# Optimization experiments

Hardware: AMD Instinct MI355X
Metric: run time of the kernel (lower is better)

Reference implementation:

```python
import jax, jax.numpy as jnp
import numpy as np

N_EVENTS = 16
N_SAMPLES = 2 ** 15  # 32768


def fft_shift(stems, shift_samples):
    """Fractionally shift each atom in time via frequency-domain phase rotation.
    stems: (B, E, N) float32; shift_samples: (B, E) float32 in [0, N].
    """
    n = stems.shape[-1]
    freqs = jnp.fft.rfftfreq(n).astype(jnp.float32)  # (n//2+1,) cycles/sample
    theta = 2.0 * jnp.pi * freqs[None, None, :] * shift_samples[..., None]  # (B,E,F)
    phase = jnp.cos(theta) - 1j * jnp.sin(theta)  # exp(-i*theta)
    spec = jnp.fft.rfft(stems, axis=-1)
    return jnp.fft.irfft(spec * phase, n=n, axis=-1)


def setup_inputs() -> dict:
    key = jax.random.key(0)
    k1, k2, k3, k4 = jax.random.split(key, 4)
    B = 64
    time_latent = jax.random.normal(k1, (B, N_EVENTS, 128), dtype=jnp.float32)
    stems = jax.random.normal(k2, (B, N_EVENTS, N_SAMPLES), dtype=jnp.float32)
    targets = jax.random.normal(k3, (B, 1, N_SAMPLES), dtype=jnp.float32)
    W_pos = jax.random.normal(k4, (1, 128), dtype=jnp.float32) * 0.1
    b_pos = jnp.zeros((1,), dtype=jnp.float32)
    return {"time_latent": time_latent, "stems": stems, "targets": targets,
            "W_pos": W_pos, "b_pos": b_pos}


def reference(time_latent, stems, targets, W_pos, b_pos):
    # to_pos: Linear(128 -> 1), then sigmoid -> fractional positions in [0,1]
    pos = jax.nn.sigmoid(jnp.einsum('bed,od->beo', time_latent, W_pos) + b_pos)
    pos = pos.reshape(-1, N_EVENTS)  # (B, E)
    # schedule_atoms: place each stem at fractional offset pos * n_samples, sum events
    shifted = fft_shift(stems, pos * N_SAMPLES)  # (B, E, N)
    scheduled = jnp.sum(shifted, axis=1, keepdims=True)  # (B, 1, N), same shape as targets
    return scheduled
```

## Files before the change

kernel.cpp:

```cpp
#include <hip/hip_runtime.h>
#include <math.h>

#define NS      32768
#define M       16384
#define NEV     16
#define NB      64
#define T2      1024

__device__ __forceinline__ int ldsIdx(int i) { return i + (i >> 5) + (i >> 10); }
#define LDS_ELEMS (M + M / 32 + M / 1024)

__device__ __forceinline__ float2 cmul(float2 a, float2 b) {
    return make_float2(a.x * b.x - a.y * b.y, a.x * b.y + a.y * b.x);
}

__device__ __forceinline__ int rev4_14(int i) {
    int r = 0;
#pragma unroll
    for (int d = 0; d < 7; ++d) { r = (r << 2) | (i & 3); i >>= 2; }
    return r;
}

__device__ __forceinline__ float2 shift_phase(int k, int si, float sf) {
    unsigned ksi = ((unsigned)k * (unsigned)si) & (unsigned)(NS - 1);
    float total = (float)ksi + (float)k * sf;
    float f = total * (1.0f / (float)NS);
    f -= floorf(f);
    float ang = -6.28318530717958647692f * f;
    float sv, cv;
    __sincosf(ang, &sv, &cv);
    return make_float2(cv, sv);
}

__device__ __forceinline__ float2 wNS(int k) {
    float ang = (float)k * (-6.28318530717958647692f / (float)NS);
    float sv, cv;
    __sincosf(ang, &sv, &cv);
    return make_float2(cv, sv);
}

__device__ __constant__ float R16C[4] = {1.0f, 0.92387953251128675613f,
                                         0.70710678118654752440f, 0.38268343236508977173f};
__device__ __constant__ float R16S[4] = {0.0f, 0.38268343236508977173f,
                                         0.70710678118654752440f, 0.92387953251128675613f};

__device__ __constant__ float C32[16] = {
    1.0f, 0.98078528040323044913f, 0.92387953251128675613f, 0.83146961230254523708f,
    0.70710678118654752440f, 0.55557023301960222474f, 0.38268343236508977173f,
    0.19509032201612826785f, 0.0f, -0.19509032201612826785f, -0.38268343236508977173f,
    -0.55557023301960222474f, -0.70710678118654752440f, -0.83146961230254523708f,
    -0.92387953251128675613f, -0.98078528040323044913f};
__device__ __constant__ float S32[16] = {
    0.0f, 0.19509032201612826785f, 0.38268343236508977173f, 0.55557023301960222474f,
    0.70710678118654752440f, 0.83146961230254523708f, 0.92387953251128675613f,
    0.98078528040323044913f, 1.0f, 0.98078528040323044913f, 0.92387953251128675613f,
    0.83146961230254523708f, 0.70710678118654752440f, 0.55557023301960222474f,
    0.38268343236508977173f, 0.19509032201612826785f};

template <int SIGN>
__device__ void fft_lds(float2* lds, int tid) {
    const float TP = (SIGN < 0) ? -6.28318530717958647692f
                                :  6.28318530717958647692f;
#pragma unroll
    for (int tp = 0; tp < 3; ++tp) {
        const int t = 2 * tp;
        const int q = 1 << (2 * t);
        const int j = tid & (q - 1);
        const int base = ((tid >> (2 * t)) << (2 * t + 4)) + j;
        float2 x[16];
#pragma unroll
        for (int l = 0; l < 16; ++l) x[l] = lds[ldsIdx(base + l * q)];

        float2 ww, w1, w2, w3;
        if (tp > 0) {
            float sv, cv;
            __sincosf(TP * (float)j / (float)(16 * q), &sv, &cv);
            ww = make_float2(cv, sv);
            float2 s2 = cmul(ww, ww);
            w1 = cmul(s2, s2);
            w2 = cmul(w1, w1);
            w3 = cmul(w2, w1);
        }

#pragma unroll
        for (int m = 0; m < 4; ++m) {
            float2 a0 = x[4 * m], a1 = x[4 * m + 1], a2 = x[4 * m + 2], a3 = x[4 * m + 3];
            if (tp > 0) { a1 = cmul(a1, w1); a2 = cmul(a2, w2); a3 = cmul(a3, w3); }
            float2 u0 = make_float2(a0.x + a2.x, a0.y + a2.y);
            float2 u1 = make_float2(a0.x - a2.x, a0.y - a2.y);
            float2 u2 = make_float2(a1.x + a3.x, a1.y + a3.y);
            float2 u3 = make_float2(a1.x - a3.x, a1.y - a3.y);
            x[4 * m]     = make_float2(u0.x + u2.x, u0.y + u2.y);
            x[4 * m + 2] = make_float2(u0.x - u2.x, u0.y - u2.y);
            if (SIGN < 0) {
                x[4 * m + 1] = make_float2(u1.x + u3.y, u1.y - u3.x);
                x[4 * m + 3] = make_float2(u1.x - u3.y, u1.y + u3.x);
            } else {
                x[4 * m + 1] = make_float2(u1.x - u3.y, u1.y + u3.x);
                x[4 * m + 3] = make_float2(u1.x + u3.y, u1.y - u3.x);
            }
        }

#pragma unroll
        for (int n = 0; n < 4; ++n) {
            float2 a0 = x[n], a1 = x[n + 4], a2 = x[n + 8], a3 = x[n + 12];
            if (!(tp == 0 && n == 0)) {
                float2 r = make_float2(R16C[n], (SIGN < 0) ? -R16S[n] : R16S[n]);
                float2 wp = (tp > 0) ? ((n > 0) ? cmul(ww, r) : ww) : r;
                float2 wp2 = cmul(wp, wp);
                float2 wp3 = cmul(wp2, wp);
                a1 = cmul(a1, wp);
                a2 = cmul(a2, wp2);
                a3 = cmul(a3, wp3);
            }
            float2 u0 = make_float2(a0.x + a2.x, a0.y + a2.y);
            float2 u1 = make_float2(a0.x - a2.x, a0.y - a2.y);
            float2 u2 = make_float2(a1.x + a3.x, a1.y + a3.y);
            float2 u3 = make_float2(a1.x - a3.x, a1.y - a3.y);
            x[n]      = make_float2(u0.x + u2.x, u0.y + u2.y);
            x[n + 8]  = make_float2(u0.x - u2.x, u0.y - u2.y);
            if (SIGN < 0) {
                x[n + 4]  = make_float2(u1.x + u3.y, u1.y - u3.x);
                x[n + 12] = make_float2(u1.x - u3.y, u1.y + u3.x);
            } else {
                x[n + 4]  = make_float2(u1.x - u3.y, u1.y + u3.x);
                x[n + 12] = make_float2(u1.x + u3.y, u1.y - u3.x);
            }
        }
#pragma unroll
        for (int l = 0; l < 16; ++l) lds[ldsIdx(base + l * q)] = x[l];
        __syncthreads();
    }

    {
        const int q = 4096;
        const float c = TP / (float)(4 * q);
        float sv, cv;
        __sincosf(c * (float)tid, &sv, &cv);
        const float2 w1b = make_float2(cv, sv);
#pragma unroll
        for (int it = 0; it < (M / 4) / T2; ++it) {
            const int j = tid + it * T2;
            float2 w1;
            if (it == 0) w1 = w1b;
            else {
                float2 rot = make_float2(R16C[it], (SIGN < 0) ? -R16S[it] : R16S[it]);
                w1 = cmul(w1b, rot);
            }
            float2 w2 = cmul(w1, w1);
            float2 w3 = cmul(w2, w1);
            const int I0 = ldsIdx(j);
            const int I1 = ldsIdx(j + q);
            const int I2 = ldsIdx(j + 2 * q);
            const int I3 = ldsIdx(j + 3 * q);
            float2 a0 = lds[I0];
            float2 a1 = cmul(lds[I1], w1);
            float2 a2 = cmul(lds[I2], w2);
            float2 a3 = cmul(lds[I3], w3);
            float2 u0 = make_float2(a0.x + a2.x, a0.y + a2.y);
            float2 u1 = make_float2(a0.x - a2.x, a0.y - a2.y);
            float2 u2 = make_float2(a1.x + a3.x, a1.y + a3.y);
            float2 u3 = make_float2(a1.x - a3.x, a1.y - a3.y);
            lds[I0] = make_float2(u0.x + u2.x, u0.y + u2.y);
            lds[I2] = make_float2(u0.x - u2.x, u0.y - u2.y);
            if (SIGN < 0) {
                lds[I1] = make_float2(u1.x + u3.y, u1.y - u3.x);
                lds[I3] = make_float2(u1.x - u3.y, u1.y + u3.x);
            } else {
                lds[I1] = make_float2(u1.x - u3.y, u1.y + u3.x);
                lds[I3] = make_float2(u1.x + u3.y, u1.y - u3.x);
            }
        }
        __syncthreads();
    }
}

__global__ __launch_bounds__(64) void pos_kernel(const float* __restrict__ tl,
                                                 const float* __restrict__ W,
                                                 const float* __restrict__ bp,
                                                 float* __restrict__ shifts) {
    int bid = blockIdx.x;
    int t = threadIdx.x;
    const float* row = tl + (size_t)bid * 128;
    float p = row[t] * W[t] + row[t + 64] * W[t + 64];
#pragma unroll
    for (int off = 32; off > 0; off >>= 1) p += __shfl_down(p, off);
    if (t == 0) {
        float x = p + bp[0];
        float sig = 1.0f / (1.0f + expf(-x));
        shifts[bid] = sig * (float)NS;
    }
}

__global__ __launch_bounds__(T2) void fft_phase_kernel(float* __restrict__ stems,
                                                       const float* __restrict__ shifts) {
    __shared__ float2 lds[LDS_ELEMS];
    const int tid = threadIdx.x;
    const int row = blockIdx.x;

    float* rowp = stems + (size_t)row * NS;
    const float4* src = (const float4*)rowp;
#pragma unroll
    for (int it = 0; it < (M / 2) / T2; ++it) {
        int i = tid + it * T2;
        float4 v = src[i];
        lds[ldsIdx(rev4_14(2 * i))]     = make_float2(v.x, v.y);
        lds[ldsIdx(rev4_14(2 * i + 1))] = make_float2(v.z, v.w);
    }
    __syncthreads();

    fft_lds<-1>(lds, tid);

    const float s = shifts[row];
    const int si = (int)floorf(s);
    const float sf = s - (float)si;
    float2* spec = (float2*)rowp;

    const float2 ph0 = shift_phase(tid, si, sf);
    const float2 w0  = wNS(tid);
    const float2 q1  = shift_phase(1024, si, sf);
    const float2 q2  = cmul(q1, q1);
    const float2 q3  = cmul(q2, q1);
    const float2 q4  = cmul(q2, q2);
    float2 phb = ph0;
#pragma unroll
    for (int t = 0; t < M / T2; ++t) {
        int k = tid + (t << 10);
        float2 ph;
        switch (t & 3) {
            case 0:  ph = phb; break;
            case 1:  ph = cmul(phb, q1); break;
            case 2:  ph = cmul(phb, q2); break;
            default: ph = cmul(phb, q3); break;
        }
        if (k == 0) {
            float2 z0 = lds[ldsIdx(0)];
            float X0 = z0.x + z0.y;
            float XM = z0.x - z0.y;
            float2 phM = shift_phase(M, si, sf);
            spec[0] = make_float2(X0, XM * phM.x);
        } else {
            float2 Zk = lds[ldsIdx(k)];
            float2 Zr = lds[ldsIdx(M - k)];
            float2 E = make_float2(0.5f * (Zk.x + Zr.x), 0.5f * (Zk.y - Zr.y));
            float2 O = make_float2(0.5f * (Zk.y + Zr.y), -0.5f * (Zk.x - Zr.x));
            float2 w = cmul(w0, make_float2(C32[t], -S32[t]));
            float2 wo = cmul(w, O);
            float2 X = make_float2(E.x + wo.x, E.y + wo.y);
            spec[k] = cmul(X, ph);
        }
        if ((t & 3) == 3) phb = cmul(phb, q4);
    }
}

__global__ __launch_bounds__(256) void reduce_kernel(const float4* __restrict__ stems,
                                                     float4* __restrict__ out) {
    int gid = blockIdx.x * 256 + threadIdx.x;
    int b = gid >> 13;
    int i = gid & (NS / 4 - 1);
    const float4* base = stems + (size_t)b * NEV * (NS / 4) + i;
    float4 s = base[0];
#pragma unroll
    for (int e = 1; e < NEV; ++e) {
        float4 v = base[(size_t)e * (NS / 4)];
        s.x += v.x; s.y += v.y; s.z += v.z; s.w += v.w;
    }
    out[gid] = s;
}

__global__ __launch_bounds__(T2) void inv_kernel(float* __restrict__ out) {
    __shared__ float2 lds[LDS_ELEMS];
    const int tid = threadIdx.x;
    const int b = blockIdx.x;

    const float4* src = (const float4*)(out + (size_t)b * NS);
#pragma unroll
    for (int it = 0; it < (M / 2) / T2; ++it) {
        int i = tid + it * T2;
        float4 v = src[i];
        lds[ldsIdx(rev4_14(2 * i))]     = make_float2(v.x, v.y);
        lds[ldsIdx(rev4_14(2 * i + 1))] = make_float2(v.z, v.w);
    }
    __syncthreads();

    const float2 w0 = wNS(tid);
#pragma unroll
    for (int t = 0; t < (M / 2) / T2; ++t) {
        int k = tid + (t << 10);
        if (k == 0) {
            float2 a0 = lds[ldsIdx(0)];
            lds[ldsIdx(0)] = make_float2(0.5f * (a0.x + a0.y), 0.5f * (a0.x - a0.y));
            int rh = ldsIdx(rev4_14(M / 2));
            float2 ah = lds[rh];
            lds[rh] = make_float2(ah.x, -ah.y);
        } else {
            int pk = ldsIdx(rev4_14(k));
            int pm = ldsIdx(rev4_14(M - k));
            float2 a = lds[pk];
            float2 bb = lds[pm];
            float2 w = cmul(w0, make_float2(C32[t], -S32[t]));
            float2 E1 = make_float2(0.5f * (a.x + bb.x), 0.5f * (a.y - bb.y));
            float2 D1 = make_float2(0.5f * (a.x - bb.x), 0.5f * (a.y + bb.y));
            float2 wc = make_float2(w.x, -w.y);
            float2 O1 = cmul(wc, D1);
            float2 z1 = make_float2(E1.x - O1.y, E1.y + O1.x);
            float2 E2 = make_float2(E1.x, -E1.y);
            float2 D2 = make_float2(-D1.x, D1.y);
            float2 O2 = cmul(w, D2);
            O2 = make_float2(-O2.x, -O2.y);
            float2 z2 = make_float2(E2.x - O2.y, E2.y + O2.x);
            lds[pk] = z1;
            lds[pm] = z2;
        }
    }
    __syncthreads();

    fft_lds<1>(lds, tid);

    const float invM = 1.0f / (float)M;
    float4* dst = (float4*)(out + (size_t)b * NS);
#pragma unroll
    for (int it = 0; it < (NS / 4) / T2; ++it) {
        int i = tid + it * T2;
        float2 z0 = lds[ldsIdx(2 * i)];
        float2 z1 = lds[ldsIdx(2 * i + 1)];
        dst[i] = make_float4(z0.x * invM, z0.y * invM, z1.x * invM, z1.y * invM);
    }
}

extern "C" void kernel_launch(void* const* d_in, const int* in_sizes, int n_in,
                              void* d_out, int out_size, void* d_ws, size_t ws_size,
                              hipStream_t stream) {
    const float* time_latent = (const float*)d_in[0];
    float* stems = (float*)d_in[1];
    const float* W_pos = (const float*)d_in[3];
    const float* b_pos = (const float*)d_in[4];
    float* out = (float*)d_out;

    float* shifts = (float*)d_ws;

    pos_kernel<<<NB * NEV, 64, 0, stream>>>(time_latent, W_pos, b_pos, shifts);
    fft_phase_kernel<<<NB * NEV, T2, 0, stream>>>(stems, shifts);
    reduce_kernel<<<(NB * NS / 4) / 256, 256, 0, stream>>>((const float4*)stems,
                                                           (float4*)out);
    inv_kernel<<<NB, T2, 0, stream>>>(out);
}
```

Baseline: 296.6 us.

## Fuse pos into FFT kernel, fold first radix-4 stage into load, move repack into reduce

The position linear layer and sigmoid are computed inside the forward FFT kernel, which removes one launch and the round trip of shifts through global memory. The first radix-4 stage is done in registers during the global load and bit-reversed scatter, so the FFT runs as three radix-16 passes instead of three radix-16 passes plus a separate radix-4 LDS pass. The inverse real-FFT pre-twiddle (z-pair repack) moves out of the inverse kernel, which runs only 64 blocks, and into the reduce kernel, which also reads mirrored elements from global memory. In exchange the reduce kernel does strided mirrored reads, and the restructured FFT stage ordering must stay correct.

```diff
diff --git a/kernel.cpp b/kernel.cpp
--- a/kernel.cpp
+++ b/kernel.cpp
@@ -58,12 +58,52 @@
     0.38268343236508977173f, 0.19509032201612826785f};
 
 template <int SIGN>
-__device__ void fft_lds(float2* lds, int tid) {
+__device__ __forceinline__ void btf4(float2* a) {
+    float2 a0 = a[0], a1 = a[1], a2 = a[2], a3 = a[3];
+    float2 u0 = make_float2(a0.x + a2.x, a0.y + a2.y);
+    float2 u1 = make_float2(a0.x - a2.x, a0.y - a2.y);
+    float2 u2 = make_float2(a1.x + a3.x, a1.y + a3.y);
+    float2 u3 = make_float2(a1.x - a3.x, a1.y - a3.y);
+    a[0] = make_float2(u0.x + u2.x, u0.y + u2.y);
+    a[2] = make_float2(u0.x - u2.x, u0.y - u2.y);
+    if (SIGN < 0) {
+        a[1] = make_float2(u1.x + u3.y, u1.y - u3.x);
+        a[3] = make_float2(u1.x - u3.y, u1.y + u3.x);
+    } else {
+        a[1] = make_float2(u1.x - u3.y, u1.y + u3.x);
+        a[3] = make_float2(u1.x + u3.y, u1.y - u3.x);
+    }
+}
+
+template <int SIGN>
+__device__ __forceinline__ void load_stage0_scatter(const float4* __restrict__ src,
+                                                    float2* lds, int tid) {
+    const int R = rev4_14(2 * tid);
+    float2 g0[4], g1[4], g2[4], g3[4];
+#pragma unroll
+    for (int it = 0; it < 8; ++it) {
+        float4 v = src[tid + (it << 10)];
+        int l = it >> 1;
+        if ((it & 1) == 0) { g0[l] = make_float2(v.x, v.y); g1[l] = make_float2(v.z, v.w); }
+        else               { g2[l] = make_float2(v.x, v.y); g3[l] = make_float2(v.z, v.w); }
+    }
+    btf4<SIGN>(g0); btf4<SIGN>(g1); btf4<SIGN>(g2); btf4<SIGN>(g3);
+#pragma unroll
+    for (int l = 0; l < 4; ++l) {
+        lds[ldsIdx(R + l)]               = g0[l];
+        lds[ldsIdx(R + 4096 + l)]        = g1[l];
+        lds[ldsIdx(R + 8 + l)]           = g2[l];
+        lds[ldsIdx(R + 8 + 4096 + l)]    = g3[l];
+    }
+}
+
+template <int SIGN>
+__device__ void fft_pairs(float2* lds, int tid) {
     const float TP = (SIGN < 0) ? -6.28318530717958647692f
                                 :  6.28318530717958647692f;
 #pragma unroll
     for (int tp = 0; tp < 3; ++tp) {
-        const int t = 2 * tp;
+        const int t = 2 * tp + 1;
         const int q = 1 << (2 * t);
         const int j = tid & (q - 1);
         const int base = ((tid >> (2 * t)) << (2 * t + 4)) + j;
@@ -71,21 +111,18 @@
 #pragma unroll
         for (int l = 0; l < 16; ++l) x[l] = lds[ldsIdx(base + l * q)];
 
-        float2 ww, w1, w2, w3;
-        if (tp > 0) {
-            float sv, cv;
-            __sincosf(TP * (float)j / (float)(16 * q), &sv, &cv);
-            ww = make_float2(cv, sv);
-            float2 s2 = cmul(ww, ww);
-            w1 = cmul(s2, s2);
-            w2 = cmul(w1, w1);
-            w3 = cmul(w2, w1);
-        }
+        float sv, cv;
+        __sincosf(TP * (float)j / (float)(16 * q), &sv, &cv);
+        float2 ww = make_float2(cv, sv);
+        float2 s2 = cmul(ww, ww);
+        float2 w1 = cmul(s2, s2);
+        float2 w2 = cmul(w1, w1);
+        float2 w3 = cmul(w2, w1);
 
 #pragma unroll
         for (int m = 0; m < 4; ++m) {
             float2 a0 = x[4 * m], a1 = x[4 * m + 1], a2 = x[4 * m + 2], a3 = x[4 * m + 3];
-            if (tp > 0) { a1 = cmul(a1, w1); a2 = cmul(a2, w2); a3 = cmul(a3, w3); }
+            a1 = cmul(a1, w1); a2 = cmul(a2, w2); a3 = cmul(a3, w3);
             float2 u0 = make_float2(a0.x + a2.x, a0.y + a2.y);
             float2 u1 = make_float2(a0.x - a2.x, a0.y - a2.y);
             float2 u2 = make_float2(a1.x + a3.x, a1.y + a3.y);
@@ -104,9 +141,9 @@
 #pragma unroll
         for (int n = 0; n < 4; ++n) {
             float2 a0 = x[n], a1 = x[n + 4], a2 = x[n + 8], a3 = x[n + 12];
-            if (!(tp == 0 && n == 0)) {
+            {
                 float2 r = make_float2(R16C[n], (SIGN < 0) ? -R16S[n] : R16S[n]);
-                float2 wp = (tp > 0) ? ((n > 0) ? cmul(ww, r) : ww) : r;
+                float2 wp = (n > 0) ? cmul(ww, r) : ww;
                 float2 wp2 = cmul(wp, wp);
                 float2 wp3 = cmul(wp2, wp);
                 a1 = cmul(a1, wp);
@@ -131,87 +168,34 @@
         for (int l = 0; l < 16; ++l) lds[ldsIdx(base + l * q)] = x[l];
         __syncthreads();
     }
-
-    {
-        const int q = 4096;
-        const float c = TP / (float)(4 * q);
-        float sv, cv;
-        __sincosf(c * (float)tid, &sv, &cv);
-        const float2 w1b = make_float2(cv, sv);
-#pragma unroll
-        for (int it = 0; it < (M / 4) / T2; ++it) {
-            const int j = tid + it * T2;
-            float2 w1;
-            if (it == 0) w1 = w1b;
-            else {
-                float2 rot = make_float2(R16C[it], (SIGN < 0) ? -R16S[it] : R16S[it]);
-                w1 = cmul(w1b, rot);
-            }
-            float2 w2 = cmul(w1, w1);
-            float2 w3 = cmul(w2, w1);
-            const int I0 = ldsIdx(j);
-            const int I1 = ldsIdx(j + q);
-            const int I2 = ldsIdx(j + 2 * q);
-            const int I3 = ldsIdx(j + 3 * q);
-            float2 a0 = lds[I0];
-            float2 a1 = cmul(lds[I1], w1);
-            float2 a2 = cmul(lds[I2], w2);
-            float2 a3 = cmul(lds[I3], w3);
-            float2 u0 = make_float2(a0.x + a2.x, a0.y + a2.y);
-            float2 u1 = make_float2(a0.x - a2.x, a0.y - a2.y);
-            float2 u2 = make_float2(a1.x + a3.x, a1.y + a3.y);
-            float2 u3 = make_float2(a1.x - a3.x, a1.y - a3.y);
-            lds[I0] = make_float2(u0.x + u2.x, u0.y + u2.y);
-            lds[I2] = make_float2(u0.x - u2.x, u0.y - u2.y);
-            if (SIGN < 0) {
-                lds[I1] = make_float2(u1.x + u3.y, u1.y - u3.x);
-                lds[I3] = make_float2(u1.x - u3.y, u1.y + u3.x);
-            } else {
-                lds[I1] = make_float2(u1.x - u3.y, u1.y + u3.x);
-                lds[I3] = make_float2(u1.x + u3.y, u1.y - u3.x);
-            }
-        }
-        __syncthreads();
-    }
-}
-
-__global__ __launch_bounds__(64) void pos_kernel(const float* __restrict__ tl,
-                                                 const float* __restrict__ W,
-                                                 const float* __restrict__ bp,
-                                                 float* __restrict__ shifts) {
-    int bid = blockIdx.x;
-    int t = threadIdx.x;
-    const float* row = tl + (size_t)bid * 128;
-    float p = row[t] * W[t] + row[t + 64] * W[t + 64];
-#pragma unroll
-    for (int off = 32; off > 0; off >>= 1) p += __shfl_down(p, off);
-    if (t == 0) {
-        float x = p + bp[0];
-        float sig = 1.0f / (1.0f + expf(-x));
-        shifts[bid] = sig * (float)NS;
-    }
 }
 
 __global__ __launch_bounds__(T2) void fft_phase_kernel(float* __restrict__ stems,
-                                                       const float* __restrict__ shifts) {
+                                                       const float* __restrict__ tl,
+                                                       const float* __restrict__ W,
+                                                       const float* __restrict__ bp) {
     __shared__ float2 lds[LDS_ELEMS];
+    __shared__ float sh_shift;
     const int tid = threadIdx.x;
     const int row = blockIdx.x;
-
     float* rowp = stems + (size_t)row * NS;
-    const float4* src = (const float4*)rowp;
-#pragma unroll
-    for (int it = 0; it < (M / 2) / T2; ++it) {
-        int i = tid + it * T2;
-        float4 v = src[i];
-        lds[ldsIdx(rev4_14(2 * i))]     = make_float2(v.x, v.y);
-        lds[ldsIdx(rev4_14(2 * i + 1))] = make_float2(v.z, v.w);
-    }
+
+    if (tid < 64) {
+        const float* trow = tl + (size_t)row * 128;
+        float p = trow[tid] * W[tid] + trow[tid + 64] * W[tid + 64];
+#pragma unroll
+        for (int off = 32; off > 0; off >>= 1) p += __shfl_down(p, off);
+        if (tid == 0) {
+            float x = p + bp[0];
+            sh_shift = (1.0f / (1.0f + expf(-x))) * (float)NS;
+        }
+    }
+
+    load_stage0_scatter<-1>((const float4*)rowp, lds, tid);
     __syncthreads();
-
-    fft_lds<-1>(lds, tid);
-
-    const float s = shifts[row];
+    fft_pairs<-1>(lds, tid);
+
+    const float s = sh_shift;
     const int si = (int)floorf(s);
     const float sf = s - (float)si;
     float2* spec = (float2*)rowp;
@@ -253,72 +237,76 @@
     }
 }
 
-__global__ __launch_bounds__(256) void reduce_kernel(const float4* __restrict__ stems,
-                                                     float4* __restrict__ out) {
+__device__ __forceinline__ void zpair(float2 a, float2 bb, float2 w,
+                                      float2* z1, float2* z2) {
+    float2 E1 = make_float2(0.5f * (a.x + bb.x), 0.5f * (a.y - bb.y));
+    float2 D1 = make_float2(0.5f * (a.x - bb.x), 0.5f * (a.y + bb.y));
+    float2 O1 = cmul(make_float2(w.x, -w.y), D1);
+    *z1 = make_float2(E1.x - O1.y, E1.y + O1.x);
+    float2 D2 = make_float2(-D1.x, D1.y);
+    float2 O2p = cmul(w, D2);
+    *z2 = make_float2(E1.x + O2p.y, -E1.y - O2p.x);
+}
+
+__global__ __launch_bounds__(256) void reduce_repack(const float* __restrict__ stems,
+                                                     float* __restrict__ out) {
     int gid = blockIdx.x * 256 + threadIdx.x;
-    int b = gid >> 13;
-    int i = gid & (NS / 4 - 1);
-    const float4* base = stems + (size_t)b * NEV * (NS / 4) + i;
-    float4 s = base[0];
-#pragma unroll
-    for (int e = 1; e < NEV; ++e) {
-        float4 v = base[(size_t)e * (NS / 4)];
-        s.x += v.x; s.y += v.y; s.z += v.z; s.w += v.w;
-    }
-    out[gid] = s;
+    int b = gid >> 12;
+    int i = gid & 4095;
+    const float* brow = stems + (size_t)b * NEV * NS;
+    float4 sA = make_float4(0.f, 0.f, 0.f, 0.f);
+    float2 sP1 = make_float2(0.f, 0.f);
+    float2 sP2 = make_float2(0.f, 0.f);
+    float2 sH  = make_float2(0.f, 0.f);
+#pragma unroll
+    for (int e = 0; e < NEV; ++e) {
+        const float* rp = brow + (size_t)e * NS;
+        float4 va = ((const float4*)rp)[i];
+        sA.x += va.x; sA.y += va.y; sA.z += va.z; sA.w += va.w;
+        if (i) {
+            float2 p1 = ((const float2*)rp)[M - 2 * i - 1];
+            float2 p2 = ((const float2*)rp)[M - 2 * i];
+            sP1.x += p1.x; sP1.y += p1.y;
+            sP2.x += p2.x; sP2.y += p2.y;
+        } else {
+            float2 p1 = ((const float2*)rp)[M - 1];
+            float2 h  = ((const float2*)rp)[M / 2];
+            sP1.x += p1.x; sP1.y += p1.y;
+            sH.x  += h.x;  sH.y  += h.y;
+        }
+    }
+    float* orow = out + (size_t)b * NS;
+    float2* o2 = (float2*)orow;
+    if (i) {
+        int k = 2 * i;
+        float2 z1a, z2a, z1b, z2b;
+        zpair(make_float2(sA.x, sA.y), sP2, wNS(k),     &z1a, &z2a);
+        zpair(make_float2(sA.z, sA.w), sP1, wNS(k + 1), &z1b, &z2b);
+        ((float4*)orow)[i] = make_float4(z1a.x, z1a.y, z1b.x, z1b.y);
+        o2[M - k]     = z2a;
+        o2[M - k - 1] = z2b;
+    } else {
+        float2 z0 = make_float2(0.5f * (sA.x + sA.y), 0.5f * (sA.x - sA.y));
+        float2 z1b, z2b;
+        zpair(make_float2(sA.z, sA.w), sP1, wNS(1), &z1b, &z2b);
+        ((float4*)orow)[0] = make_float4(z0.x, z0.y, z1b.x, z1b.y);
+        o2[M - 1] = z2b;
+        o2[M / 2] = make_float2(sH.x, -sH.y);
+    }
 }
 
 __global__ __launch_bounds__(T2) void inv_kernel(float* __restrict__ out) {
     __shared__ float2 lds[LDS_ELEMS];
     const int tid = threadIdx.x;
     const int b = blockIdx.x;
-
-    const float4* src = (const float4*)(out + (size_t)b * NS);
-#pragma unroll
-    for (int it = 0; it < (M / 2) / T2; ++it) {
-        int i = tid + it * T2;
-        float4 v = src[i];
-        lds[ldsIdx(rev4_14(2 * i))]     = make_float2(v.x, v.y);
-        lds[ldsIdx(rev4_14(2 * i + 1))] = make_float2(v.z, v.w);
-    }
+    float* rowp = out + (size_t)b * NS;
+
+    load_stage0_scatter<1>((const float4*)rowp, lds, tid);
     __syncthreads();
-
-    const float2 w0 = wNS(tid);
-#pragma unroll
-    for (int t = 0; t < (M / 2) / T2; ++t) {
-        int k = tid + (t << 10);
-        if (k == 0) {
-            float2 a0 = lds[ldsIdx(0)];
-            lds[ldsIdx(0)] = make_float2(0.5f * (a0.x + a0.y), 0.5f * (a0.x - a0.y));
-            int rh = ldsIdx(rev4_14(M / 2));
-            float2 ah = lds[rh];
-            lds[rh] = make_float2(ah.x, -ah.y);
-        } else {
-            int pk = ldsIdx(rev4_14(k));
-            int pm = ldsIdx(rev4_14(M - k));
-            float2 a = lds[pk];
-            float2 bb = lds[pm];
-            float2 w = cmul(w0, make_float2(C32[t], -S32[t]));
-            float2 E1 = make_float2(0.5f * (a.x + bb.x), 0.5f * (a.y - bb.y));
-            float2 D1 = make_float2(0.5f * (a.x - bb.x), 0.5f * (a.y + bb.y));
-            float2 wc = make_float2(w.x, -w.y);
-            float2 O1 = cmul(wc, D1);
-            float2 z1 = make_float2(E1.x - O1.y, E1.y + O1.x);
-            float2 E2 = make_float2(E1.x, -E1.y);
-            float2 D2 = make_float2(-D1.x, D1.y);
-            float2 O2 = cmul(w, D2);
-            O2 = make_float2(-O2.x, -O2.y);
-            float2 z2 = make_float2(E2.x - O2.y, E2.y + O2.x);
-            lds[pk] = z1;
-            lds[pm] = z2;
-        }
-    }
-    __syncthreads();
-
-    fft_lds<1>(lds, tid);
+    fft_pairs<1>(lds, tid);
 
     const float invM = 1.0f / (float)M;
-    float4* dst = (float4*)(out + (size_t)b * NS);
+    float4* dst = (float4*)rowp;
 #pragma unroll
     for (int it = 0; it < (NS / 4) / T2; ++it) {
         int i = tid + it * T2;
@@ -337,11 +325,7 @@
     const float* b_pos = (const float*)d_in[4];
     float* out = (float*)d_out;
 
-    float* shifts = (float*)d_ws;
-
-    pos_kernel<<<NB * NEV, 64, 0, stream>>>(time_latent, W_pos, b_pos, shifts);
-    fft_phase_kernel<<<NB * NEV, T2, 0, stream>>>(stems, shifts);
-    reduce_kernel<<<(NB * NS / 4) / 256, 256, 0, stream>>>((const float4*)stems,
-                                                           (float4*)out);
+    fft_phase_kernel<<<NB * NEV, T2, 0, stream>>>(stems, time_latent, W_pos, b_pos);
+    reduce_repack<<<(NB * (M / 4)) / 256, 256, 0, stream>>>(stems, out);
     inv_kernel<<<NB, T2, 0, stream>>>(out);
 }
```

Result: faster. 286.7 us (-3.3%).
